# Kernel tuning notes

Measured on AMD Instinct MI355X. Metric: run time of the kernel, lower is better.

Reference implementation:

```python
import jax, jax.numpy as jnp
import numpy as np

N_BITS = 8
LEVELS = 2 ** N_BITS - 1  # 255 quantization levels (asymmetric uniform)
EPS = 1e-8


def _round_ste(x):
    # straight-through round (forward: round, backward: identity)
    return x + jax.lax.stop_gradient(jnp.round(x) - x)


def _fake_quant_uniform(x):
    # dynamic per-tensor asymmetric uniform quantization (UniformQuantizer)
    xmin = jnp.min(x)
    xmax = jnp.max(x)
    scale = jnp.maximum((xmax - xmin) / LEVELS, EPS)
    zero_point = jnp.round(-xmin / scale)
    x_int = jnp.clip(_round_ste(x / scale) + zero_point, 0, LEVELS)
    return (x_int - zero_point) * scale


def setup_inputs() -> dict:
    key = jax.random.key(0)
    kA, kB = jax.random.split(key)
    A = jax.random.normal(kA, (4, 4096, 4096), dtype=jnp.float32)  # [batch, M, K]
    B = jax.random.normal(kB, (4096, 4096), dtype=jnp.float32)     # [K, N]
    return {"A": A, "B": B}


def reference(A, B):
    # QuantMatMul.forward with use_input_quant=True, use_weight_quant=True
    Aq = _fake_quant_uniform(A)
    Bq = _fake_quant_uniform(B)
    return Aq @ Bq  # [batch, M, N]
```

## Files before the change

kernel.cpp:

```cpp
#include <hip/hip_runtime.h>


#define K_DIM 4096
#define N_COLS 4096
#define M_ROWS 16384

typedef __attribute__((ext_vector_type(4))) int int4v;
typedef __attribute__((ext_vector_type(16))) int int16v;

static const size_t OFF_AQ = 0;
static const size_t OFF_BT = (size_t)64 << 20;
static const size_t OFF_RS = OFF_BT + ((size_t)16 << 20);
static const size_t OFF_CS = OFF_RS + (size_t)M_ROWS * 4;
static const size_t OFF_MM = OFF_CS + (size_t)N_COLS * 4;

__device__ __forceinline__ unsigned enc_f(float f) {
  unsigned u = __float_as_uint(f);
  return (u & 0x80000000u) ? ~u : (u | 0x80000000u);
}
__device__ __forceinline__ float dec_f(unsigned e) {
  unsigned u = (e & 0x80000000u) ? (e & 0x7fffffffu) : ~e;
  return __uint_as_float(u);
}

__device__ __forceinline__ int quantize1(float x, float r, float zp) {
  return (int)(fminf(fmaxf(rintf(x * r) + zp, 0.0f), 255.0f)) - 128;
}

__device__ __forceinline__ void gload16(const void* g, void* l) {
  __builtin_amdgcn_global_load_lds(
      (const __attribute__((address_space(1))) unsigned int*)g,
      (__attribute__((address_space(3))) unsigned int*)l, 16, 0, 0);
}

__device__ __forceinline__ void qparams_a(const unsigned* mm, float& ra, float& zpa) {
  const float amin = dec_f(mm[0]), amax = dec_f(mm[1]);
  const float sa = fmaxf((amax - amin) / 255.0f, 1e-8f);
  zpa = rintf(-amin / sa);
  ra = 1.0f / sa;
}
__device__ __forceinline__ void qparams_b(const unsigned* mm, float& rb, float& zpb) {
  const float bmin = dec_f(mm[2]), bmax = dec_f(mm[3]);
  const float sb = fmaxf((bmax - bmin) / 255.0f, 1e-8f);
  zpb = rintf(-bmin / sb);
  rb = 1.0f / sb;
}

__global__ __launch_bounds__(256) void init_k(unsigned* __restrict__ mm,
                                              int* __restrict__ colsum) {
  const int i = blockIdx.x * 256 + threadIdx.x;
  if (i < N_COLS) colsum[i] = 0;
  if (i == N_COLS) {
    mm[0] = 0xFFFFFFFFu; mm[1] = 0u;
    mm[2] = 0xFFFFFFFFu; mm[3] = 0u;
  }
}

__global__ __launch_bounds__(256) void minmax_k(const float4* __restrict__ A,
                                                const float4* __restrict__ B,
                                                unsigned* __restrict__ mm) {
  const bool isB = blockIdx.x >= 4096;
  const float4* __restrict__ x = isB ? B : A;
  const long n4 = isB ? (long)K_DIM * N_COLS / 4 : (long)M_ROWS * K_DIM / 4;
  const int nblk = isB ? 1024 : 4096;
  const int bid = isB ? (int)blockIdx.x - 4096 : (int)blockIdx.x;
  unsigned* m = mm + (isB ? 2 : 0);

  float lo = 3.402823466e38f, hi = -3.402823466e38f;
  long i = (long)bid * blockDim.x + threadIdx.x;
  const long stride = (long)nblk * blockDim.x;
  for (; i < n4; i += stride) {
    float4 v = x[i];
    lo = fminf(lo, fminf(fminf(v.x, v.y), fminf(v.z, v.w)));
    hi = fmaxf(hi, fmaxf(fmaxf(v.x, v.y), fmaxf(v.z, v.w)));
  }
  for (int off = 32; off; off >>= 1) {
    lo = fminf(lo, __shfl_down(lo, off));
    hi = fmaxf(hi, __shfl_down(hi, off));
  }
  __shared__ float slo[4], shi[4];
  const int t = threadIdx.x;
  if ((t & 63) == 0) { slo[t >> 6] = lo; shi[t >> 6] = hi; }
  __syncthreads();
  if (t == 0) {
    for (int w = 1; w < 4; w++) { lo = fminf(lo, slo[w]); hi = fmaxf(hi, shi[w]); }
    atomicMin(&m[0], enc_f(lo));
    atomicMax(&m[1], enc_f(hi));
  }
}

__global__ __launch_bounds__(256) void quantA_k(const float* __restrict__ A,
                                                signed char* __restrict__ Aq,
                                                int* __restrict__ rowsum,
                                                const unsigned* __restrict__ mm) {
  float ra, zpa;
  qparams_a(mm, ra, zpa);
  const int row = blockIdx.x, t = threadIdx.x;
  const float4* src = (const float4*)(A + (size_t)row * K_DIM);
  unsigned* dst = (unsigned*)(Aq + (size_t)row * K_DIM);
  int sum = 0;
#pragma unroll
  for (int j = 0; j < 4; j++) {
    const int d = j * 256 + t;
    float4 v = src[d];
    int q0 = quantize1(v.x, ra, zpa);
    int q1 = quantize1(v.y, ra, zpa);
    int q2 = quantize1(v.z, ra, zpa);
    int q3 = quantize1(v.w, ra, zpa);
    sum += q0 + q1 + q2 + q3;
    dst[d] = ((unsigned)q0 & 255u) | (((unsigned)q1 & 255u) << 8) |
             (((unsigned)q2 & 255u) << 16) | (((unsigned)q3 & 255u) << 24);
  }
  for (int off = 32; off; off >>= 1) sum += __shfl_down(sum, off);
  __shared__ int sw[4];
  if ((t & 63) == 0) sw[t >> 6] = sum;
  __syncthreads();
  if (t == 0) rowsum[row] = sw[0] + sw[1] + sw[2] + sw[3];
}

__global__ __launch_bounds__(256) void quantB_k(const float* __restrict__ B,
                                                signed char* __restrict__ Bt,
                                                int* __restrict__ colsum,
                                                const unsigned* __restrict__ mm) {
  float rb, zpb;
  qparams_b(mm, rb, zpb);
  __shared__ unsigned char s[64][72];
  const int n0 = blockIdx.x * 64, k0 = blockIdx.y * 64;
  const int t = threadIdx.x;
  const int kr = t >> 2, tl = t & 3;
  const float* rowp = B + (size_t)(k0 + kr) * N_COLS + n0;
#pragma unroll
  for (int j = 0; j < 4; j++) {
    const int fi = tl + j * 4;
    float4 v = *(const float4*)(rowp + fi * 4);
    int q0 = quantize1(v.x, rb, zpb);
    int q1 = quantize1(v.y, rb, zpb);
    int q2 = quantize1(v.z, rb, zpb);
    int q3 = quantize1(v.w, rb, zpb);
    *(unsigned*)&s[kr][fi * 4] = ((unsigned)q0 & 255u) | (((unsigned)q1 & 255u) << 8) |
                                 (((unsigned)q2 & 255u) << 16) | (((unsigned)q3 & 255u) << 24);
  }
  __syncthreads();
  const int nr = t >> 2;
  const int kb = tl * 16;
  unsigned w[4];
  int psum = 0;
#pragma unroll
  for (int jj = 0; jj < 4; jj++) {
    unsigned b0 = s[kb + jj * 4 + 0][nr];
    unsigned b1 = s[kb + jj * 4 + 1][nr];
    unsigned b2 = s[kb + jj * 4 + 2][nr];
    unsigned b3 = s[kb + jj * 4 + 3][nr];
    w[jj] = b0 | (b1 << 8) | (b2 << 16) | (b3 << 24);
    psum += (int)(signed char)b0 + (int)(signed char)b1 +
            (int)(signed char)b2 + (int)(signed char)b3;
  }
  int4v o = {(int)w[0], (int)w[1], (int)w[2], (int)w[3]};
  *(int4v*)(Bt + (size_t)(n0 + nr) * K_DIM + (k0 + kb)) = o;
  psum += __shfl_xor(psum, 1);
  psum += __shfl_xor(psum, 2);
  if (tl == 0) atomicAdd(&colsum[n0 + nr], psum);
}

__global__ __launch_bounds__(512, 4) void gemm_k(const signed char* __restrict__ Aq,
                                                 const signed char* __restrict__ Bt,
                                                 float* __restrict__ C,
                                                 const int* __restrict__ rowsum,
                                                 const int* __restrict__ colsum,
                                                 const unsigned* __restrict__ mm) {
  __shared__ signed char lds[73728];
  const int t = threadIdx.x;

  const int orig = blockIdx.x;
  const int wgid = (orig & 7) * 256 + (orig >> 3);
  const int m0 = (wgid >> 5) * 256;
  const int n0 = (wgid & 31) * 128;

  const int w = t >> 6, l = t & 63;
  const int wm16 = (w >> 1) * 16;
  const int wn16 = (w & 1) * 16;
  const int r32 = l & 31, h = l >> 5;
  const int u = r32 >> 2, c4 = (r32 & 3) * 4;

  unsigned aAddr[2][2], bAddr[2][2];
#pragma unroll
  for (int mi = 0; mi < 2; ++mi)
#pragma unroll
    for (int kk = 0; kk < 2; ++kk)
      aAddr[mi][kk] = (unsigned)(wm16 + 8 * mi + u) * 256 +
                      ((unsigned)((c4 + 2 * kk + h) ^ u) << 4);
#pragma unroll
  for (int ni = 0; ni < 2; ++ni)
#pragma unroll
    for (int kk = 0; kk < 2; ++kk)
      bAddr[ni][kk] = 16384u + (unsigned)(wn16 + 8 * ni + u) * 256 +
                      ((unsigned)((c4 + 2 * kk + h) ^ u) << 4);

  const int bs_ = t & 15, Rq = t >> 4;
  const int b16 = bs_ ^ (Rq & 7);
  const int sc = b16 >> 2, slb = b16 & 3;
  const signed char* pA0 = Aq + (size_t)(m0 + 4 * Rq + sc) * K_DIM + slb * 16;
  const signed char* pA1 = pA0 + (size_t)128 * K_DIM;
  const signed char* pB  = Bt + (size_t)(n0 + 4 * Rq + sc) * K_DIM + slb * 16;

  int16v acc[2][2] = {};

#define STAGE(SO) do {                                    \
    gload16(pA0, lds + (SO) + t * 16);                    \
    gload16(pA1, lds + (SO) + 8192 + t * 16);             \
    gload16(pB,  lds + (SO) + 16384 + t * 16);            \
    pA0 += 64; pA1 += 64; pB += 64; } while (0)

#define MM_(A, B, CC) CC = __builtin_amdgcn_mfma_i32_32x32x32_i8(A, B, CC, 0, 0, 0)

#define COMP(SO) do {                                                 \
    int4v b0 = *(const int4v*)(lds + (SO) + bAddr[0][0]);             \
    int4v b1 = *(const int4v*)(lds + (SO) + bAddr[1][0]);             \
    int4v a0 = *(const int4v*)(lds + (SO) + aAddr[0][0]);             \
    int4v a1 = *(const int4v*)(lds + (SO) + aAddr[1][0]);             \
    __builtin_amdgcn_s_setprio(1);                                    \
    MM_(a0, b0, acc[0][0]); MM_(a0, b1, acc[0][1]);                   \
    MM_(a1, b0, acc[1][0]); MM_(a1, b1, acc[1][1]);                   \
    __builtin_amdgcn_s_setprio(0);                                    \
    b0 = *(const int4v*)(lds + (SO) + bAddr[0][1]);                   \
    b1 = *(const int4v*)(lds + (SO) + bAddr[1][1]);                   \
    a0 = *(const int4v*)(lds + (SO) + aAddr[0][1]);                   \
    a1 = *(const int4v*)(lds + (SO) + aAddr[1][1]);                   \
    __builtin_amdgcn_s_setprio(1);                                    \
    MM_(a0, b0, acc[0][0]); MM_(a0, b1, acc[0][1]);                   \
    MM_(a1, b0, acc[1][0]); MM_(a1, b1, acc[1][1]);                   \
    __builtin_amdgcn_s_setprio(0);                                    \
  } while (0)

#define WAITN(N) asm volatile("s_waitcnt vmcnt(" #N ")" ::: "memory")
#define BARR do { __builtin_amdgcn_s_barrier();                       \
                  __builtin_amdgcn_sched_barrier(0); } while (0)

#define ITER(SC, SN) do { WAITN(3); BARR; STAGE(SN); COMP(SC); } while (0)

  STAGE(0);
  STAGE(24576);

#pragma unroll 1
  for (int g = 0; g < 20; ++g) {
    ITER(0, 49152);
    ITER(24576, 0);
    ITER(49152, 24576);
  }
  ITER(0, 49152);
  ITER(24576, 0);
  WAITN(3); BARR; COMP(49152);
  WAITN(0); BARR; COMP(0);

#undef STAGE
#undef MM_
#undef COMP
#undef WAITN
#undef BARR
#undef ITER

  const float amin = dec_f(mm[0]), amax = dec_f(mm[1]);
  const float bmin = dec_f(mm[2]), bmax = dec_f(mm[3]);
  const float sa = fmaxf((amax - amin) / 255.0f, 1e-8f);
  const float sb = fmaxf((bmax - bmin) / 255.0f, 1e-8f);
  const int za = (int)rintf(-amin / sa) - 128;
  const int zb = (int)rintf(-bmin / sb) - 128;
  const float sab = sa * sb;
  const int kzz = K_DIM * za * zb;
  const int wm = wm16 * 4, wn = wn16 * 4;
  const int col0 = n0 + wn + r32;
  const int cs0 = za * colsum[col0];
  const int cs1 = za * colsum[col0 + 32];
#pragma unroll
  for (int mi = 0; mi < 2; ++mi) {
    const int rbase = m0 + wm + mi * 32 + 4 * h;
#pragma unroll
    for (int r = 0; r < 16; ++r) {
      const int row = rbase + (r & 3) + 8 * (r >> 2);
      const int base = kzz - zb * rowsum[row];
      C[(size_t)row * N_COLS + col0]      = sab * (float)(acc[mi][0][r] + base - cs0);
      C[(size_t)row * N_COLS + col0 + 32] = sab * (float)(acc[mi][1][r] + base - cs1);
    }
  }
}

extern "C" void kernel_launch(void* const* d_in, const int* in_sizes, int n_in,
                              void* d_out, int out_size, void* d_ws, size_t ws_size,
                              hipStream_t stream) {
  const float* A = (const float*)d_in[0];
  const float* B = (const float*)d_in[1];
  float* C = (float*)d_out;
  char* ws = (char*)d_ws;
  signed char* Aq = (signed char*)(ws + OFF_AQ);
  signed char* Bt = (signed char*)(ws + OFF_BT);
  int* rowsum = (int*)(ws + OFF_RS);
  int* colsum = (int*)(ws + OFF_CS);
  unsigned* mm = (unsigned*)(ws + OFF_MM);

  init_k<<<17, 256, 0, stream>>>(mm, colsum);
  minmax_k<<<5120, 256, 0, stream>>>((const float4*)A, (const float4*)B, mm);
  quantA_k<<<M_ROWS, 256, 0, stream>>>(A, Aq, rowsum, mm);
  quantB_k<<<dim3(64, 64), 256, 0, stream>>>(B, Bt, colsum, mm);
  gemm_k<<<2048, 512, 0, stream>>>(Aq, Bt, C, rowsum, colsum, mm);
}
```

Before: 882.0 us.

## Halve GEMM workgroup to four waves, each computing a 4x2 MFMA tile

The int8 GEMM keeps the same 256x128 block tile but uses 256 threads instead of 512. Each wave now owns a 4x2 grid of 32x32 MFMA accumulators instead of 2x2, which raises operand reuse per LDS read and halves the number of waves competing for LDS bandwidth. All LDS fragment reads for a k-step are now issued before the global-to-LDS staging of the next stage. The MFMAs then follow, so the loads can overlap. The cost is roughly double the accumulator and operand registers per wave and fewer waves per CU to hide latency.

```diff
diff --git a/kernel.cpp b/kernel.cpp
--- a/kernel.cpp
+++ b/kernel.cpp
@@ -162,7 +162,7 @@
   if (tl == 0) atomicAdd(&colsum[n0 + nr], psum);
 }
 
-__global__ __launch_bounds__(512, 4) void gemm_k(const signed char* __restrict__ Aq,
+__global__ __launch_bounds__(256, 2) void gemm_k(const signed char* __restrict__ Aq,
                                                  const signed char* __restrict__ Bt,
                                                  float* __restrict__ C,
                                                  const int* __restrict__ rowsum,
@@ -177,58 +177,75 @@
   const int n0 = (wgid & 31) * 128;
 
   const int w = t >> 6, l = t & 63;
-  const int wm16 = (w >> 1) * 16;
-  const int wn16 = (w & 1) * 16;
+  const int wm4 = (w >> 1) * 32;
+  const int wn4 = (w & 1) * 16;
   const int r32 = l & 31, h = l >> 5;
   const int u = r32 >> 2, c4 = (r32 & 3) * 4;
 
-  unsigned aAddr[2][2], bAddr[2][2];
-#pragma unroll
-  for (int mi = 0; mi < 2; ++mi)
+  unsigned aAddr[4][2], bAddr[2][2];
+#pragma unroll
+  for (int mi = 0; mi < 4; ++mi)
 #pragma unroll
     for (int kk = 0; kk < 2; ++kk)
-      aAddr[mi][kk] = (unsigned)(wm16 + 8 * mi + u) * 256 +
+      aAddr[mi][kk] = (unsigned)(wm4 + 8 * mi + u) * 256 +
                       ((unsigned)((c4 + 2 * kk + h) ^ u) << 4);
 #pragma unroll
   for (int ni = 0; ni < 2; ++ni)
 #pragma unroll
     for (int kk = 0; kk < 2; ++kk)
-      bAddr[ni][kk] = 16384u + (unsigned)(wn16 + 8 * ni + u) * 256 +
+      bAddr[ni][kk] = 16384u + (unsigned)(wn4 + 8 * ni + u) * 256 +
                       ((unsigned)((c4 + 2 * kk + h) ^ u) << 4);
 
   const int bs_ = t & 15, Rq = t >> 4;
   const int b16 = bs_ ^ (Rq & 7);
   const int sc = b16 >> 2, slb = b16 & 3;
   const signed char* pA0 = Aq + (size_t)(m0 + 4 * Rq + sc) * K_DIM + slb * 16;
-  const signed char* pA1 = pA0 + (size_t)128 * K_DIM;
-  const signed char* pB  = Bt + (size_t)(n0 + 4 * Rq + sc) * K_DIM + slb * 16;
-
-  int16v acc[2][2] = {};
+  const signed char* pA1 = pA0 + (size_t)64 * K_DIM;
+  const signed char* pA2 = pA0 + (size_t)128 * K_DIM;
+  const signed char* pA3 = pA0 + (size_t)192 * K_DIM;
+  const signed char* pB0 = Bt + (size_t)(n0 + 4 * Rq + sc) * K_DIM + slb * 16;
+  const signed char* pB1 = pB0 + (size_t)64 * K_DIM;
+
+  int16v acc[4][2] = {};
 
 #define STAGE(SO) do {                                    \
     gload16(pA0, lds + (SO) + t * 16);                    \
-    gload16(pA1, lds + (SO) + 8192 + t * 16);             \
-    gload16(pB,  lds + (SO) + 16384 + t * 16);            \
-    pA0 += 64; pA1 += 64; pB += 64; } while (0)
+    gload16(pA1, lds + (SO) + 4096 + t * 16);             \
+    gload16(pA2, lds + (SO) + 8192 + t * 16);             \
+    gload16(pA3, lds + (SO) + 12288 + t * 16);            \
+    gload16(pB0, lds + (SO) + 16384 + t * 16);            \
+    gload16(pB1, lds + (SO) + 20480 + t * 16);            \
+    pA0 += 64; pA1 += 64; pA2 += 64; pA3 += 64;           \
+    pB0 += 64; pB1 += 64; } while (0)
 
 #define MM_(A, B, CC) CC = __builtin_amdgcn_mfma_i32_32x32x32_i8(A, B, CC, 0, 0, 0)
 
-#define COMP(SO) do {                                                 \
-    int4v b0 = *(const int4v*)(lds + (SO) + bAddr[0][0]);             \
-    int4v b1 = *(const int4v*)(lds + (SO) + bAddr[1][0]);             \
-    int4v a0 = *(const int4v*)(lds + (SO) + aAddr[0][0]);             \
-    int4v a1 = *(const int4v*)(lds + (SO) + aAddr[1][0]);             \
+#define COMP(SO, STAGING) do {                                        \
+    const signed char* sb = lds + (SO);                               \
+    int4v b00 = *(const int4v*)(sb + bAddr[0][0]);                    \
+    int4v b10 = *(const int4v*)(sb + bAddr[1][0]);                    \
+    int4v a00 = *(const int4v*)(sb + aAddr[0][0]);                    \
+    int4v a10 = *(const int4v*)(sb + aAddr[1][0]);                    \
+    int4v a20 = *(const int4v*)(sb + aAddr[2][0]);                    \
+    int4v a30 = *(const int4v*)(sb + aAddr[3][0]);                    \
+    int4v b01 = *(const int4v*)(sb + bAddr[0][1]);                    \
+    int4v b11 = *(const int4v*)(sb + bAddr[1][1]);                    \
+    int4v a01 = *(const int4v*)(sb + aAddr[0][1]);                    \
+    int4v a11 = *(const int4v*)(sb + aAddr[1][1]);                    \
+    int4v a21 = *(const int4v*)(sb + aAddr[2][1]);                    \
+    int4v a31 = *(const int4v*)(sb + aAddr[3][1]);                    \
+    STAGING;                                                          \
     __builtin_amdgcn_s_setprio(1);                                    \
-    MM_(a0, b0, acc[0][0]); MM_(a0, b1, acc[0][1]);                   \
-    MM_(a1, b0, acc[1][0]); MM_(a1, b1, acc[1][1]);                   \
+    MM_(a00, b00, acc[0][0]); MM_(a00, b10, acc[0][1]);               \
+    MM_(a10, b00, acc[1][0]); MM_(a10, b10, acc[1][1]);               \
+    MM_(a20, b00, acc[2][0]); MM_(a20, b10, acc[2][1]);               \
+    MM_(a30, b00, acc[3][0]); MM_(a30, b10, acc[3][1]);               \
     __builtin_amdgcn_s_setprio(0);                                    \
-    b0 = *(const int4v*)(lds + (SO) + bAddr[0][1]);                   \
-    b1 = *(const int4v*)(lds + (SO) + bAddr[1][1]);                   \
-    a0 = *(const int4v*)(lds + (SO) + aAddr[0][1]);                   \
-    a1 = *(const int4v*)(lds + (SO) + aAddr[1][1]);                   \
     __builtin_amdgcn_s_setprio(1);                                    \
-    MM_(a0, b0, acc[0][0]); MM_(a0, b1, acc[0][1]);                   \
-    MM_(a1, b0, acc[1][0]); MM_(a1, b1, acc[1][1]);                   \
+    MM_(a01, b01, acc[0][0]); MM_(a01, b11, acc[0][1]);               \
+    MM_(a11, b01, acc[1][0]); MM_(a11, b11, acc[1][1]);               \
+    MM_(a21, b01, acc[2][0]); MM_(a21, b11, acc[2][1]);               \
+    MM_(a31, b01, acc[3][0]); MM_(a31, b11, acc[3][1]);               \
     __builtin_amdgcn_s_setprio(0);                                    \
   } while (0)
 
@@ -236,7 +253,7 @@
 #define BARR do { __builtin_amdgcn_s_barrier();                       \
                   __builtin_amdgcn_sched_barrier(0); } while (0)
 
-#define ITER(SC, SN) do { WAITN(3); BARR; STAGE(SN); COMP(SC); } while (0)
+#define ITER(SC, SN) do { WAITN(6); BARR; COMP(SC, STAGE(SN)); } while (0)
 
   STAGE(0);
   STAGE(24576);
@@ -249,8 +266,8 @@
   }
   ITER(0, 49152);
   ITER(24576, 0);
-  WAITN(3); BARR; COMP(49152);
-  WAITN(0); BARR; COMP(0);
+  WAITN(6); BARR; COMP(49152, );
+  WAITN(0); BARR; COMP(0, );
 
 #undef STAGE
 #undef MM_
@@ -267,12 +284,12 @@
   const int zb = (int)rintf(-bmin / sb) - 128;
   const float sab = sa * sb;
   const int kzz = K_DIM * za * zb;
-  const int wm = wm16 * 4, wn = wn16 * 4;
+  const int wm = wm4 * 4, wn = wn4 * 4;
   const int col0 = n0 + wn + r32;
   const int cs0 = za * colsum[col0];
   const int cs1 = za * colsum[col0 + 32];
 #pragma unroll
-  for (int mi = 0; mi < 2; ++mi) {
+  for (int mi = 0; mi < 4; ++mi) {
     const int rbase = m0 + wm + mi * 32 + 4 * h;
 #pragma unroll
     for (int r = 0; r < 16; ++r) {
@@ -301,5 +318,5 @@
   minmax_k<<<5120, 256, 0, stream>>>((const float4*)A, (const float4*)B, mm);
   quantA_k<<<M_ROWS, 256, 0, stream>>>(A, Aq, rowsum, mm);
   quantB_k<<<dim3(64, 64), 256, 0, stream>>>(B, Bt, colsum, mm);
-  gemm_k<<<2048, 512, 0, stream>>>(Aq, Bt, C, rowsum, colsum, mm);
-}
+  gemm_k<<<2048, 256, 0, stream>>>(Aq, Bt, C, rowsum, colsum, mm);
+}
```

Measured after the change: 864.9 us. Within noise of the previous version (-1.9%).

## Enlarge GEMM tile to 256x256 with 4-stage LDS pipeline and split staging

Applied to the files above, without the earlier changes.

The int8 GEMM block tile grows from 256x128 to 256x256, so each wave computes a 128x32 sub-tile with 8 MFMAs per k-step. It also moves to a 4-stage LDS ring of 128KB, with A and B global loads issued in separate half-steps between barriers. The goal is to raise arithmetic intensity and cut redundant global/LDS traffic per MFMA, and to hide memory latency better. In exchange, occupancy drops to 2 blocks per CU, there are more barriers per iteration, and register pressure from 8 accumulators rises.

```diff
diff --git a/kernel.cpp b/kernel.cpp
--- a/kernel.cpp
+++ b/kernel.cpp
@@ -162,38 +162,38 @@
   if (tl == 0) atomicAdd(&colsum[n0 + nr], psum);
 }
 
-__global__ __launch_bounds__(512, 4) void gemm_k(const signed char* __restrict__ Aq,
+__global__ __launch_bounds__(512, 2) void gemm_k(const signed char* __restrict__ Aq,
                                                  const signed char* __restrict__ Bt,
                                                  float* __restrict__ C,
                                                  const int* __restrict__ rowsum,
                                                  const int* __restrict__ colsum,
                                                  const unsigned* __restrict__ mm) {
-  __shared__ signed char lds[73728];
+  __shared__ signed char lds[131072];
   const int t = threadIdx.x;
 
   const int orig = blockIdx.x;
-  const int wgid = (orig & 7) * 256 + (orig >> 3);
-  const int m0 = (wgid >> 5) * 256;
-  const int n0 = (wgid & 31) * 128;
+  const int wgid = (orig & 7) * 128 + (orig >> 3);
+  const int m0 = (wgid >> 4) * 256;
+  const int n0 = (wgid & 15) * 256;
 
   const int w = t >> 6, l = t & 63;
-  const int wm16 = (w >> 1) * 16;
-  const int wn16 = (w & 1) * 16;
+  const int wm4 = (w >> 2) * 32;
+  const int wn4 = (w & 3) * 16;
   const int r32 = l & 31, h = l >> 5;
   const int u = r32 >> 2, c4 = (r32 & 3) * 4;
 
-  unsigned aAddr[2][2], bAddr[2][2];
-#pragma unroll
-  for (int mi = 0; mi < 2; ++mi)
+  unsigned aAddr[4][2], bAddr[2][2];
+#pragma unroll
+  for (int mi = 0; mi < 4; ++mi)
 #pragma unroll
     for (int kk = 0; kk < 2; ++kk)
-      aAddr[mi][kk] = (unsigned)(wm16 + 8 * mi + u) * 256 +
+      aAddr[mi][kk] = (unsigned)(wm4 + 8 * mi + u) * 256 +
                       ((unsigned)((c4 + 2 * kk + h) ^ u) << 4);
 #pragma unroll
   for (int ni = 0; ni < 2; ++ni)
 #pragma unroll
     for (int kk = 0; kk < 2; ++kk)
-      bAddr[ni][kk] = 16384u + (unsigned)(wn16 + 8 * ni + u) * 256 +
+      bAddr[ni][kk] = 16384u + (unsigned)(wn4 + 8 * ni + u) * 256 +
                       ((unsigned)((c4 + 2 * kk + h) ^ u) << 4);
 
   const int bs_ = t & 15, Rq = t >> 4;
@@ -201,63 +201,78 @@
   const int sc = b16 >> 2, slb = b16 & 3;
   const signed char* pA0 = Aq + (size_t)(m0 + 4 * Rq + sc) * K_DIM + slb * 16;
   const signed char* pA1 = pA0 + (size_t)128 * K_DIM;
-  const signed char* pB  = Bt + (size_t)(n0 + 4 * Rq + sc) * K_DIM + slb * 16;
-
-  int16v acc[2][2] = {};
-
-#define STAGE(SO) do {                                    \
-    gload16(pA0, lds + (SO) + t * 16);                    \
-    gload16(pA1, lds + (SO) + 8192 + t * 16);             \
-    gload16(pB,  lds + (SO) + 16384 + t * 16);            \
-    pA0 += 64; pA1 += 64; pB += 64; } while (0)
+  const signed char* pB0 = Bt + (size_t)(n0 + 4 * Rq + sc) * K_DIM + slb * 16;
+  const signed char* pB1 = pB0 + (size_t)128 * K_DIM;
+
+  int16v acc[4][2] = {};
+
+#define STAGE_A(SN) do {                                  \
+    gload16(pA0, lds + (SN) + t * 16);                    \
+    gload16(pA1, lds + (SN) + 8192 + t * 16);             \
+    pA0 += 64; pA1 += 64; } while (0)
+#define STAGE_B(SN) do {                                  \
+    gload16(pB0, lds + (SN) + 16384 + t * 16);            \
+    gload16(pB1, lds + (SN) + 24576 + t * 16);            \
+    pB0 += 64; pB1 += 64; } while (0)
 
 #define MM_(A, B, CC) CC = __builtin_amdgcn_mfma_i32_32x32x32_i8(A, B, CC, 0, 0, 0)
 
-#define COMP(SO) do {                                                 \
-    int4v b0 = *(const int4v*)(lds + (SO) + bAddr[0][0]);             \
-    int4v b1 = *(const int4v*)(lds + (SO) + bAddr[1][0]);             \
-    int4v a0 = *(const int4v*)(lds + (SO) + aAddr[0][0]);             \
-    int4v a1 = *(const int4v*)(lds + (SO) + aAddr[1][0]);             \
-    __builtin_amdgcn_s_setprio(1);                                    \
-    MM_(a0, b0, acc[0][0]); MM_(a0, b1, acc[0][1]);                   \
-    MM_(a1, b0, acc[1][0]); MM_(a1, b1, acc[1][1]);                   \
-    __builtin_amdgcn_s_setprio(0);                                    \
-    b0 = *(const int4v*)(lds + (SO) + bAddr[0][1]);                   \
-    b1 = *(const int4v*)(lds + (SO) + bAddr[1][1]);                   \
-    a0 = *(const int4v*)(lds + (SO) + aAddr[0][1]);                   \
-    a1 = *(const int4v*)(lds + (SO) + aAddr[1][1]);                   \
-    __builtin_amdgcn_s_setprio(1);                                    \
-    MM_(a0, b0, acc[0][0]); MM_(a0, b1, acc[0][1]);                   \
-    MM_(a1, b0, acc[1][0]); MM_(a1, b1, acc[1][1]);                   \
-    __builtin_amdgcn_s_setprio(0);                                    \
+#define RD6(SC, KK)                                                  \
+    int4v b0 = *(const int4v*)(lds + (SC) + bAddr[0][KK]);           \
+    int4v b1 = *(const int4v*)(lds + (SC) + bAddr[1][KK]);           \
+    int4v a0 = *(const int4v*)(lds + (SC) + aAddr[0][KK]);           \
+    int4v a1 = *(const int4v*)(lds + (SC) + aAddr[1][KK]);           \
+    int4v a2 = *(const int4v*)(lds + (SC) + aAddr[2][KK]);           \
+    int4v a3 = *(const int4v*)(lds + (SC) + aAddr[3][KK]);
+
+#define MFMA8                                                        \
+    __builtin_amdgcn_s_setprio(1);                                   \
+    MM_(a0, b0, acc[0][0]); MM_(a0, b1, acc[0][1]);                  \
+    MM_(a1, b0, acc[1][0]); MM_(a1, b1, acc[1][1]);                  \
+    MM_(a2, b0, acc[2][0]); MM_(a2, b1, acc[2][1]);                  \
+    MM_(a3, b0, acc[3][0]); MM_(a3, b1, acc[3][1]);                  \
+    __builtin_amdgcn_s_setprio(0);
+
+#define WAITN(N) asm volatile("s_waitcnt vmcnt(" #N ")" ::: "memory")
+#define SBAR do { __builtin_amdgcn_sched_barrier(0);                 \
+                  __builtin_amdgcn_s_barrier();                      \
+                  __builtin_amdgcn_sched_barrier(0); } while (0)
+
+#define HALF(SC, SN, ENDW) do {                                      \
+    { RD6(SC, 0) STAGE_A(SN); SBAR; MFMA8 } SBAR;                    \
+    { RD6(SC, 1) STAGE_B(SN); SBAR; MFMA8 } ENDW; SBAR;              \
   } while (0)
-
-#define WAITN(N) asm volatile("s_waitcnt vmcnt(" #N ")" ::: "memory")
-#define BARR do { __builtin_amdgcn_s_barrier();                       \
-                  __builtin_amdgcn_sched_barrier(0); } while (0)
-
-#define ITER(SC, SN) do { WAITN(3); BARR; STAGE(SN); COMP(SC); } while (0)
-
-  STAGE(0);
-  STAGE(24576);
+#define HALF_NS(SC, ENDW) do {                                       \
+    { RD6(SC, 0) SBAR; MFMA8 } SBAR;                                 \
+    { RD6(SC, 1) SBAR; MFMA8 } ENDW; SBAR;                           \
+  } while (0)
+
+  STAGE_A(0);     STAGE_B(0);
+  STAGE_A(32768); STAGE_B(32768);
+  STAGE_A(65536); STAGE_B(65536);
+  WAITN(8); SBAR;
 
 #pragma unroll 1
-  for (int g = 0; g < 20; ++g) {
-    ITER(0, 49152);
-    ITER(24576, 0);
-    ITER(49152, 24576);
-  }
-  ITER(0, 49152);
-  ITER(24576, 0);
-  WAITN(3); BARR; COMP(49152);
-  WAITN(0); BARR; COMP(0);
-
-#undef STAGE
+  for (int g = 0; g < 15; ++g) {
+    HALF(0,     98304, WAITN(8));
+    HALF(32768, 0,     WAITN(8));
+    HALF(65536, 32768, WAITN(8));
+    HALF(98304, 65536, WAITN(8));
+  }
+  HALF(0, 98304, WAITN(8));
+  HALF_NS(32768, WAITN(4));
+  HALF_NS(65536, WAITN(0));
+  HALF_NS(98304, );
+
+#undef STAGE_A
+#undef STAGE_B
 #undef MM_
-#undef COMP
+#undef RD6
+#undef MFMA8
 #undef WAITN
-#undef BARR
-#undef ITER
+#undef SBAR
+#undef HALF
+#undef HALF_NS
 
   const float amin = dec_f(mm[0]), amax = dec_f(mm[1]);
   const float bmin = dec_f(mm[2]), bmax = dec_f(mm[3]);
@@ -267,12 +282,12 @@
   const int zb = (int)rintf(-bmin / sb) - 128;
   const float sab = sa * sb;
   const int kzz = K_DIM * za * zb;
-  const int wm = wm16 * 4, wn = wn16 * 4;
+  const int wm = wm4 * 4, wn = wn4 * 4;
   const int col0 = n0 + wn + r32;
   const int cs0 = za * colsum[col0];
   const int cs1 = za * colsum[col0 + 32];
 #pragma unroll
-  for (int mi = 0; mi < 2; ++mi) {
+  for (int mi = 0; mi < 4; ++mi) {
     const int rbase = m0 + wm + mi * 32 + 4 * h;
 #pragma unroll
     for (int r = 0; r < 16; ++r) {
@@ -301,5 +316,5 @@
   minmax_k<<<5120, 256, 0, stream>>>((const float4*)A, (const float4*)B, mm);
   quantA_k<<<M_ROWS, 256, 0, stream>>>(A, Aq, rowsum, mm);
   quantB_k<<<dim3(64, 64), 256, 0, stream>>>(B, Bt, colsum, mm);
-  gemm_k<<<2048, 512, 0, stream>>>(Aq, Bt, C, rowsum, colsum, mm);
-}
+  gemm_k<<<1024, 512, 0, stream>>>(Aq, Bt, C, rowsum, colsum, mm);
+}
```

Result: faster. 851.9 us (-3.4%).
